# Kernel tuning notes

Measured on AMD Instinct MI355X. Metric: run time of the kernel, lower is better.

## Reference

```python
import jax, jax.numpy as jnp
import numpy as np
from jax.scipy.special import logsumexp

EPS = 1e-12  # torch F.normalize eps
SINKHORN_ITERS = 3


def _l2norm(a, axis):
    n = jnp.sqrt(jnp.sum(a * a, axis=axis, keepdims=True))
    return a / jnp.maximum(n, EPS)


def _log_optimal_transport(scores, alpha, iters):
    # scores: [B, m, n]; alpha: scalar dust-bin param
    b, m, n = scores.shape
    bins = jnp.broadcast_to(alpha, (b, 1, n)).astype(scores.dtype)
    Z = jnp.concatenate([scores, bins], axis=1)  # [B, m+1, n]
    norm = -np.log(float(m + n))
    log_mu = jnp.asarray(
        np.concatenate([np.full(m, norm), [np.log(float(n - m)) + norm]]),
        scores.dtype,
    )  # [m+1]
    log_nu = jnp.full((n,), norm, scores.dtype)
    u = jnp.zeros((b, m + 1), scores.dtype)
    v = jnp.zeros((b, n), scores.dtype)
    for _ in range(iters):
        u = log_mu[None, :] - logsumexp(Z + v[:, None, :], axis=2)
        v = log_nu[None, :] - logsumexp(Z + u[:, :, None], axis=1)
    return Z + u[:, :, None] + v[:, None, :] - norm


def _forward(x, t, tw1, tb1, tw2, tb2, cw1, cb1, cw2, cb2, sw1, sb1, sw2, sb2, dust_bin):
    B, C = x.shape[0], x.shape[1]
    xf = x.reshape(B, C, -1)  # [B, C, N], 1x1 convs act per-location
    # cluster features f: [B, l, N]
    h = jax.nn.relu(jnp.einsum('oc,bcn->bon', cw1, xf) + cb1[None, :, None])
    f = jnp.einsum('oc,bcn->bon', cw2, h) + cb2[None, :, None]
    # global token: [B, g]
    tok = jax.nn.relu(t @ tw1.T + tb1) @ tw2.T + tb2
    # assignment scores p: [B, m, N]
    hs = jax.nn.relu(jnp.einsum('oc,bcn->bon', sw1, xf) + sb1[None, :, None])
    p = jnp.einsum('oc,bcn->bon', sw2, hs) + sb2[None, :, None]
    Z = _log_optimal_transport(p, dust_bin, SINKHORN_ITERS)
    P = jnp.exp(Z)[:, :-1, :]  # drop dust bin row -> [B, m, N]
    # VLAD-style aggregation: the repeat/multiply/sum is just a batched matmul
    agg = jnp.einsum('bln,bmn->blm', f, P)  # [B, l, m]
    agg = _l2norm(agg, axis=1).reshape(B, -1)  # intra-normalize over l, flatten l-major
    out = jnp.concatenate([_l2norm(tok, axis=-1), agg], axis=-1)
    return _l2norm(out, axis=-1)


def setup_inputs() -> dict:
    key = jax.random.key(0)
    ks = jax.random.split(key, 14)
    B, C, H, W = 64, 768, 32, 32
    L, M, G, HID = 128, 64, 256, 512

    def p(k, shape):
        return jax.random.normal(k, shape, jnp.float32) * 0.02

    return {
        'x': jax.random.normal(ks[0], (B, C, H, W), jnp.float32),
        't': jax.random.normal(ks[1], (B, C), jnp.float32),
        'tw1': p(ks[2], (HID, C)), 'tb1': jnp.zeros((HID,), jnp.float32),
        'tw2': p(ks[3], (G, HID)), 'tb2': jnp.zeros((G,), jnp.float32),
        'cw1': p(ks[4], (HID, C)), 'cb1': jnp.zeros((HID,), jnp.float32),
        'cw2': p(ks[5], (L, HID)), 'cb2': jnp.zeros((L,), jnp.float32),
        'sw1': p(ks[6], (HID, C)), 'sb1': jnp.zeros((HID,), jnp.float32),
        'sw2': p(ks[7], (M, HID)), 'sb2': jnp.zeros((M,), jnp.float32),
        'dust_bin': jnp.asarray(1.0, jnp.float32),
    }


def reference(x, t, tw1, tb1, tw2, tb2, cw1, cb1, cw2, cb2, sw1, sb1, sw2, sb2, dust_bin):
    return _forward(x, t, tw1, tb1, tw2, tb2, cw1, cb1, cw2, cb2, sw1, sb1, sw2, sb2, dust_bin)
```

## Files before the change

kernel.cpp:

```cpp
#include <hip/hip_runtime.h>
#include <math.h>


#define B_SZ   64
#define C_IN   768
#define N_LOC  1024
#define HID    512
#define L_DIM  128
#define M_DIM  64
#define G_DIM  256

typedef unsigned short u16;
typedef __bf16 bf16x8 __attribute__((ext_vector_type(8)));
typedef float f32x4 __attribute__((ext_vector_type(4)));

typedef const __attribute__((address_space(1))) void* gptr_t;
typedef __attribute__((address_space(3))) void* sptr_t;

__device__ __forceinline__ void load_lds16(const void* g, void* l) {
    __builtin_amdgcn_global_load_lds((gptr_t)g, (sptr_t)l, 16, 0, 0);
}

__device__ __forceinline__ u16 f2bf(float f) {
    unsigned u = __float_as_uint(f);
    u += 0x7fffu + ((u >> 16) & 1u);
    return (u16)(u >> 16);
}
__device__ __forceinline__ float bf2f(u16 h) {
    return __uint_as_float(((unsigned)h) << 16);
}

__device__ __forceinline__ float waveReduceSum(float v) {
#pragma unroll
    for (int off = 32; off > 0; off >>= 1) v += __shfl_xor(v, off, 64);
    return v;
}

__global__ __launch_bounds__(256) void prep_weights(
        const float* __restrict__ cw1, const float* __restrict__ sw1,
        const float* __restrict__ cw2, const float* __restrict__ sw2,
        u16* __restrict__ cw1p, u16* __restrict__ sw1p,
        u16* __restrict__ cw2p, u16* __restrict__ sw2p) {
    const int q = blockIdx.x * 256 + threadIdx.x;
    const float* src;
    u16* dst;
    if (q < 98304) {
        int path = q / 49152, r = q % 49152;
        int kch = r / 512, c = r & 511;
        src = (path ? sw1 : cw1) + (size_t)c * C_IN + kch * 8;
        dst = (path ? sw1p : cw1p) + (size_t)r * 8;
    } else {
        int q2 = q - 98304;
        int path = (q2 >= 8192) ? 1 : 0;
        int r = q2 - (path ? 8192 : 0);
        int S2 = path ? M_DIM : L_DIM;
        int k2 = r / (4 * S2), kc = (r / S2) & 3, c = r % S2;
        src = (path ? sw2 : cw2) + (size_t)c * HID + k2 * 32 + kc * 8;
        dst = (path ? sw2p : cw2p) + (size_t)r * 8;
    }
    float4 v0 = *(const float4*)(src);
    float4 v1 = *(const float4*)(src + 4);
    *(ushort4*)(dst) = make_ushort4(f2bf(v0.x), f2bf(v0.y), f2bf(v0.z), f2bf(v0.w));
    *(ushort4*)(dst + 4) = make_ushort4(f2bf(v1.x), f2bf(v1.y), f2bf(v1.z), f2bf(v1.w));
}

__global__ __launch_bounds__(256) void transpose_x(const float* __restrict__ x,
                                                   u16* __restrict__ xP) {
    __shared__ float tile[64][65];
    const int n0 = blockIdx.x * 64;
    const int c0 = blockIdx.y * 64;
    const size_t b = blockIdx.z;
    const float* xb = x + b * (size_t)(C_IN * N_LOC);
    u16* xpb = xP + b * (size_t)(N_LOC * C_IN);
    const int tid = threadIdx.x;

    const int jn = (tid & 15) * 4;
    const int cr = tid >> 4;
#pragma unroll
    for (int r = 0; r < 4; ++r) {
        int c = cr + r * 16;
        float4 v = *(const float4*)(xb + (size_t)(c0 + c) * N_LOC + n0 + jn);
        tile[c][jn + 0] = v.x;
        tile[c][jn + 1] = v.y;
        tile[c][jn + 2] = v.z;
        tile[c][jn + 3] = v.w;
    }
    __syncthreads();

    const int n = tid & 63;
    const int ch0 = tid >> 6;
    const int nG = n0 + n;
#pragma unroll
    for (int r = 0; r < 2; ++r) {
        const int ch = ch0 + r * 4;
        const int cG = c0 + ch * 8;
        u16* dst = xpb + (size_t)(nG >> 6) * (64 * C_IN) + (cG >> 5) * 2048 +
                   ((cG & 31) >> 3) * 512 + (nG & 63) * 8;
        ushort4 o0 = make_ushort4(f2bf(tile[ch * 8 + 0][n]), f2bf(tile[ch * 8 + 1][n]),
                                  f2bf(tile[ch * 8 + 2][n]), f2bf(tile[ch * 8 + 3][n]));
        ushort4 o1 = make_ushort4(f2bf(tile[ch * 8 + 4][n]), f2bf(tile[ch * 8 + 5][n]),
                                  f2bf(tile[ch * 8 + 6][n]), f2bf(tile[ch * 8 + 7][n]));
        *(ushort4*)(dst) = o0;
        *(ushort4*)(dst + 4) = o1;
    }
}

__global__ __launch_bounds__(256, 2) void fused12(
        const u16* __restrict__ xP,
        const u16* __restrict__ cw1p, const float* __restrict__ cb1,
        const u16* __restrict__ cw2p, const float* __restrict__ cb2,
        const u16* __restrict__ sw1p, const float* __restrict__ sb1,
        const u16* __restrict__ sw2p, const float* __restrict__ sb2,
        u16* __restrict__ fT, u16* __restrict__ pT) {
    __shared__ __align__(16) u16 LDSu[36864];
    const int tid = threadIdx.x;
    const int lane = tid & 63;
    const int wc = tid >> 6;

    const int id = blockIdx.x + 16 * blockIdx.y + 32 * blockIdx.z;
    const int nid = (id & 7) * 256 + (id >> 3);
    const int bx = nid & 15;
    const int path = (nid >> 4) & 1;
    const int bz = nid >> 5;
    const int r0 = bx * 64;

    const u16* W1p = path ? sw1p : cw1p;
    const float* B1 = path ? sb1 : cb1;
    const u16* W2p = path ? sw2p : cw2p;
    const float* B2 = path ? sb2 : cb2;
    u16* O2 = path ? pT : fT;
    const int S2 = path ? M_DIM : L_DIM;

    const u16* Ap = xP + (size_t)bz * N_LOC * C_IN + (size_t)bx * (64 * C_IN);

    f32x4 acc1[4][8];
#pragma unroll
    for (int mi = 0; mi < 4; ++mi)
#pragma unroll
        for (int ni = 0; ni < 8; ++ni)
            acc1[mi][ni] = (f32x4){0.f, 0.f, 0.f, 0.f};

    const int nk = C_IN / 32;

#define STG_A(db_, kt_)                                                        \
    load_lds16(Ap + (size_t)(kt_) * 2048 + tid * 8, &LDSu[(db_) * 2048 + tid * 8])
#define STG_B(db_, kt_)                                                        \
    do {                                                                       \
        _Pragma("unroll")                                                      \
        for (int j_ = 0; j_ < 8; ++j_)                                         \
            load_lds16(W1p + (size_t)(kt_) * 16384 + (size_t)(j_ * 256 + tid) * 8, \
                       &LDSu[4096 + (db_) * 16384 + (j_ * 256 + tid) * 8]);    \
    } while (0)

#define AV_PTR(db_, mi_)                                                       \
    ((const bf16x8*)&LDSu[(db_) * 2048 + (lane >> 4) * 512 +                   \
                          (16 * (mi_) + (lane & 15)) * 8])
#define BW_PTR(db_, ni_)                                                       \
    ((const bf16x8*)&LDSu[4096 + (db_) * 16384 + (lane >> 4) * 4096 +          \
                          (128 * wc + 16 * (ni_) + (lane & 15)) * 8])

    STG_A(0, 0);
    STG_B(0, 0);
    STG_A(1, 1);
    asm volatile("s_waitcnt vmcnt(1)" ::: "memory");
    __builtin_amdgcn_s_barrier();

    for (int t = 0; t < nk; ++t) {
        const int db = t & 1;
        bf16x8 av[4], bw[8];

#pragma unroll
        for (int mi = 0; mi < 4; ++mi) av[mi] = *AV_PTR(db, mi);
#pragma unroll
        for (int ni = 0; ni < 8; ++ni) bw[ni] = *BW_PTR(db, ni);
        if (t + 1 < nk) STG_B(db ^ 1, t + 1);

        asm volatile("s_waitcnt lgkmcnt(0)" ::: "memory");
        __builtin_amdgcn_sched_barrier(0);
        __builtin_amdgcn_s_barrier();

        if (t + 2 < nk) STG_A(db, t + 2);

        __builtin_amdgcn_s_setprio(1);
#pragma unroll
        for (int mi = 0; mi < 4; ++mi)
#pragma unroll
            for (int ni = 0; ni < 8; ++ni)
                acc1[mi][ni] = __builtin_amdgcn_mfma_f32_16x16x32_bf16(
                    av[mi], bw[ni], acc1[mi][ni], 0, 0, 0);
        __builtin_amdgcn_s_setprio(0);
        __builtin_amdgcn_sched_barrier(0);

        if (t + 2 < nk)
            asm volatile("s_waitcnt vmcnt(1)" ::: "memory");
        else
            asm volatile("s_waitcnt vmcnt(0)" ::: "memory");
        __builtin_amdgcn_s_barrier();
    }
#undef STG_A
#undef STG_B
#undef AV_PTR
#undef BW_PTR

    {
        float bv1[8];
#pragma unroll
        for (int ni = 0; ni < 8; ++ni)
            bv1[ni] = B1[128 * wc + 16 * ni + (lane & 15)];
#pragma unroll
        for (int mi = 0; mi < 4; ++mi)
#pragma unroll
            for (int ni = 0; ni < 8; ++ni)
#pragma unroll
                for (int rr = 0; rr < 4; ++rr) {
                    int n = 16 * mi + (lane >> 4) * 4 + rr;
                    int c = 128 * wc + 16 * ni + (lane & 15);
                    float v = fmaxf(acc1[mi][ni][rr] + bv1[ni], 0.f);
                    LDSu[(c >> 3) * 512 + n * 8 + (c & 7)] = f2bf(v);
                }
    }
    __syncthreads();

    f32x4 acc2[4][2];
#pragma unroll
    for (int mi = 0; mi < 4; ++mi) {
        acc2[mi][0] = (f32x4){0.f, 0.f, 0.f, 0.f};
        acc2[mi][1] = (f32x4){0.f, 0.f, 0.f, 0.f};
    }
    const int c2base = (S2 == L_DIM) ? 32 * wc : 16 * wc;
    const int cA = c2base + (lane & 15);
    const int cB = c2base + 16 + (lane & 15);
    const int fb0 = (lane >> 4) * S2 + cA;
    const int fb1 = (lane >> 4) * S2 + cB;

    bf16x8 w0n = *(const bf16x8*)(W2p + (size_t)fb0 * 8);
    bf16x8 w1n = {};
    if (S2 == L_DIM) w1n = *(const bf16x8*)(W2p + (size_t)fb1 * 8);

    for (int k2 = 0; k2 < 16; ++k2) {
        bf16x8 w0 = w0n, w1 = w1n;
        if (k2 < 15) {
            w0n = *(const bf16x8*)(W2p + ((size_t)(k2 + 1) * 4 * S2 + fb0) * 8);
            if (S2 == L_DIM)
                w1n = *(const bf16x8*)(W2p + ((size_t)(k2 + 1) * 4 * S2 + fb1) * 8);
        }
        bf16x8 a2[4];
#pragma unroll
        for (int mi = 0; mi < 4; ++mi)
            a2[mi] = *(const bf16x8*)&LDSu[(k2 * 4 + (lane >> 4)) * 512 +
                                           (16 * mi + (lane & 15)) * 8];
#pragma unroll
        for (int mi = 0; mi < 4; ++mi) {
            acc2[mi][0] = __builtin_amdgcn_mfma_f32_16x16x32_bf16(
                a2[mi], w0, acc2[mi][0], 0, 0, 0);
            if (S2 == L_DIM)
                acc2[mi][1] = __builtin_amdgcn_mfma_f32_16x16x32_bf16(
                    a2[mi], w1, acc2[mi][1], 0, 0, 0);
        }
    }

    const float b20 = B2[cA];
    const float b21 = (S2 == L_DIM) ? B2[cB] : 0.f;
    u16* Ob = O2 + (size_t)bz * N_LOC * S2;
#pragma unroll
    for (int mi = 0; mi < 4; ++mi)
#pragma unroll
        for (int rr = 0; rr < 4; ++rr) {
            int row = r0 + 16 * mi + (lane >> 4) * 4 + rr;
            Ob[(size_t)row * S2 + cA] = f2bf(acc2[mi][0][rr] + b20);
            if (S2 == L_DIM)
                Ob[(size_t)row * S2 + cB] = f2bf(acc2[mi][1][rr] + b21);
        }
}

__global__ __launch_bounds__(256) void tok1_kernel(const float* __restrict__ t,
                                                   const float* __restrict__ tw1,
                                                   const float* __restrict__ tb1,
                                                   float* __restrict__ hidb) {
    __shared__ __align__(16) float tl[C_IN];
    const int b = blockIdx.y;
    const int j0 = blockIdx.x * 64;
    const int tid = threadIdx.x;
    const int lane = tid & 63;
    const int wave = tid >> 6;
    for (int i = tid; i < C_IN; i += 256) tl[i] = t[(size_t)b * C_IN + i];
    __syncthreads();
    for (int j = wave; j < 64; j += 4) {
        const int row = j0 + j;
        const float4* wr = (const float4*)(tw1 + (size_t)row * C_IN);
        const float4* tr = (const float4*)tl;
        float s = 0.f;
#pragma unroll
        for (int q = 0; q < 3; ++q) {
            float4 wv = wr[lane + 64 * q];
            float4 tv = tr[lane + 64 * q];
            s += wv.x * tv.x + wv.y * tv.y + wv.z * tv.z + wv.w * tv.w;
        }
        s = waveReduceSum(s);
        if (lane == 0) hidb[(size_t)b * HID + row] = fmaxf(s + tb1[row], 0.f);
    }
}

__global__ __launch_bounds__(256) void tok2_kernel(const float* __restrict__ hidb,
                                                   const float* __restrict__ tw2,
                                                   const float* __restrict__ tb2,
                                                   float* __restrict__ tok) {
    __shared__ __align__(16) float hl[HID];
    const int b = blockIdx.y;
    const int g0 = blockIdx.x * 64;
    const int tid = threadIdx.x;
    const int lane = tid & 63;
    const int wave = tid >> 6;
    for (int i = tid; i < HID; i += 256) hl[i] = hidb[(size_t)b * HID + i];
    __syncthreads();
    for (int j = wave; j < 64; j += 4) {
        const int row = g0 + j;
        const float4* wr = (const float4*)(tw2 + (size_t)row * HID);
        const float4* hr = (const float4*)hl;
        float s = 0.f;
#pragma unroll
        for (int q = 0; q < 2; ++q) {
            float4 wv = wr[lane + 64 * q];
            float4 hv = hr[lane + 64 * q];
            s += wv.x * hv.x + wv.y * hv.y + wv.z * hv.z + wv.w * hv.w;
        }
        s = waveReduceSum(s);
        if (lane == 0) tok[(size_t)b * G_DIM + row] = s + tb2[row];
    }
}

__global__ __launch_bounds__(1024) void sinkhorn_kernel(const u16* __restrict__ pT,
                                                        const float* __restrict__ dust,
                                                        u16* __restrict__ PTb) {
    __shared__ u16 sp[M_DIM][N_LOC];
    __shared__ float eu[M_DIM + 1];
    __shared__ float ev[N_LOC];
    const int b = blockIdx.x;
    const int t = threadIdx.x;
    const int lane = t & 63;
    const int wave = t >> 6;
    const float alpha = dust[0];
    const float Ea = __expf(alpha);
    const float mu = 1.f / 1088.f;
    const float mu64 = 960.f / 1088.f;
    const float nu = 1.f / 1088.f;

    const uint4* prow = (const uint4*)(pT + ((size_t)b * N_LOC + t) * M_DIM);
#pragma unroll
    for (int q = 0; q < 8; ++q) {
        uint4 ch = prow[q];
        sp[q * 8 + 0][t] = (u16)(ch.x);
        sp[q * 8 + 1][t] = (u16)(ch.x >> 16);
        sp[q * 8 + 2][t] = (u16)(ch.y);
        sp[q * 8 + 3][t] = (u16)(ch.y >> 16);
        sp[q * 8 + 4][t] = (u16)(ch.z);
        sp[q * 8 + 5][t] = (u16)(ch.z >> 16);
        sp[q * 8 + 6][t] = (u16)(ch.w);
        sp[q * 8 + 7][t] = (u16)(ch.w >> 16);
    }
#pragma unroll
    for (int m = 0; m < M_DIM; ++m)
        sp[m][t] = f2bf(__expf(bf2f(sp[m][t])));
    ev[t] = 1.f;
    __syncthreads();

    for (int it = 0; it < 3; ++it) {
        for (int m = wave; m < M_DIM + 1; m += 16) {
            float s = 0.f;
            if (m < M_DIM) {
#pragma unroll
                for (int q = 0; q < 16; ++q) {
                    int c = lane + 64 * q;
                    s += bf2f(sp[m][c]) * ev[c];
                }
            } else {
#pragma unroll
                for (int q = 0; q < 16; ++q) {
                    int c = lane + 64 * q;
                    s += ev[c];
                }
                s *= Ea;
            }
            s = waveReduceSum(s);
            if (lane == 0) eu[m] = ((m < M_DIM) ? mu : mu64) / s;
        }
        __syncthreads();
        float s = Ea * eu[M_DIM];
#pragma unroll 8
        for (int m = 0; m < M_DIM; ++m) s += bf2f(sp[m][t]) * eu[m];
        ev[t] = nu / s;
        __syncthreads();
    }

    const float evt = ev[t] * 1088.f;
    u16* Prow = PTb + ((size_t)b * N_LOC + t) * M_DIM;
#pragma unroll
    for (int m8 = 0; m8 < M_DIM; m8 += 8) {
        unsigned v0 = f2bf(bf2f(sp[m8 + 0][t]) * eu[m8 + 0] * evt);
        unsigned v1 = f2bf(bf2f(sp[m8 + 1][t]) * eu[m8 + 1] * evt);
        unsigned v2 = f2bf(bf2f(sp[m8 + 2][t]) * eu[m8 + 2] * evt);
        unsigned v3 = f2bf(bf2f(sp[m8 + 3][t]) * eu[m8 + 3] * evt);
        unsigned v4 = f2bf(bf2f(sp[m8 + 4][t]) * eu[m8 + 4] * evt);
        unsigned v5 = f2bf(bf2f(sp[m8 + 5][t]) * eu[m8 + 5] * evt);
        unsigned v6 = f2bf(bf2f(sp[m8 + 6][t]) * eu[m8 + 6] * evt);
        unsigned v7 = f2bf(bf2f(sp[m8 + 7][t]) * eu[m8 + 7] * evt);
        uint4 w;
        w.x = v0 | (v1 << 16);
        w.y = v2 | (v3 << 16);
        w.z = v4 | (v5 << 16);
        w.w = v6 | (v7 << 16);
        *(uint4*)(Prow + m8) = w;
    }
}

__global__ __launch_bounds__(256) void agg_kernel(const u16* __restrict__ fT,
                                                  const u16* __restrict__ PTb,
                                                  float* __restrict__ agg) {
    __shared__ float Fs[64][36];
    __shared__ float Ps[64][68];
    const int b = blockIdx.y;
    const int l0 = blockIdx.x * 32;
    const int tid = threadIdx.x;
    const u16* fb = fT + (size_t)b * N_LOC * L_DIM;
    const u16* Pb = PTb + (size_t)b * N_LOC * M_DIM;

    const int sn = tid >> 2;
    const int flc = (tid & 3) * 8;
    const int pmc = (tid & 3) * 16;
    const int tl = (tid >> 4) * 2;
    const int tm = (tid & 15) * 4;

    float acc[2][4] = {};

    for (int n0 = 0; n0 < N_LOC; n0 += 64) {
        __syncthreads();
        {
            uint4 ld = *(const uint4*)(fb + (size_t)(n0 + sn) * L_DIM + l0 + flc);
            Fs[sn][flc + 0] = bf2f((u16)(ld.x));
            Fs[sn][flc + 1] = bf2f((u16)(ld.x >> 16));
            Fs[sn][flc + 2] = bf2f((u16)(ld.y));
            Fs[sn][flc + 3] = bf2f((u16)(ld.y >> 16));
            Fs[sn][flc + 4] = bf2f((u16)(ld.z));
            Fs[sn][flc + 5] = bf2f((u16)(ld.z >> 16));
            Fs[sn][flc + 6] = bf2f((u16)(ld.w));
            Fs[sn][flc + 7] = bf2f((u16)(ld.w >> 16));
        }
        {
            const u16* psrc = Pb + (size_t)(n0 + sn) * M_DIM + pmc;
            uint4 p0 = *(const uint4*)(psrc);
            uint4 p1 = *(const uint4*)(psrc + 8);
            Ps[sn][pmc + 0] = bf2f((u16)(p0.x));
            Ps[sn][pmc + 1] = bf2f((u16)(p0.x >> 16));
            Ps[sn][pmc + 2] = bf2f((u16)(p0.y));
            Ps[sn][pmc + 3] = bf2f((u16)(p0.y >> 16));
            Ps[sn][pmc + 4] = bf2f((u16)(p0.z));
            Ps[sn][pmc + 5] = bf2f((u16)(p0.z >> 16));
            Ps[sn][pmc + 6] = bf2f((u16)(p0.w));
            Ps[sn][pmc + 7] = bf2f((u16)(p0.w >> 16));
            Ps[sn][pmc + 8] = bf2f((u16)(p1.x));
            Ps[sn][pmc + 9] = bf2f((u16)(p1.x >> 16));
            Ps[sn][pmc + 10] = bf2f((u16)(p1.y));
            Ps[sn][pmc + 11] = bf2f((u16)(p1.y >> 16));
            Ps[sn][pmc + 12] = bf2f((u16)(p1.z));
            Ps[sn][pmc + 13] = bf2f((u16)(p1.z >> 16));
            Ps[sn][pmc + 14] = bf2f((u16)(p1.w));
            Ps[sn][pmc + 15] = bf2f((u16)(p1.w >> 16));
        }
        __syncthreads();
#pragma unroll 8
        for (int nn = 0; nn < 64; ++nn) {
            float a0 = Fs[nn][tl];
            float a1 = Fs[nn][tl + 1];
            float4 p4 = *(const float4*)&Ps[nn][tm];
            acc[0][0] = fmaf(a0, p4.x, acc[0][0]);
            acc[0][1] = fmaf(a0, p4.y, acc[0][1]);
            acc[0][2] = fmaf(a0, p4.z, acc[0][2]);
            acc[0][3] = fmaf(a0, p4.w, acc[0][3]);
            acc[1][0] = fmaf(a1, p4.x, acc[1][0]);
            acc[1][1] = fmaf(a1, p4.y, acc[1][1]);
            acc[1][2] = fmaf(a1, p4.z, acc[1][2]);
            acc[1][3] = fmaf(a1, p4.w, acc[1][3]);
        }
    }

#pragma unroll
    for (int i = 0; i < 2; ++i) {
        float* dst = agg + ((size_t)b * L_DIM + l0 + tl + i) * M_DIM + tm;
        *(float4*)dst = make_float4(acc[i][0], acc[i][1], acc[i][2], acc[i][3]);
    }
}

__global__ __launch_bounds__(256) void final_kernel(const float* __restrict__ agg,
                                                    const float* __restrict__ tok,
                                                    float* __restrict__ out) {
    __shared__ __align__(16) float ag[L_DIM * M_DIM];
    __shared__ float rm[M_DIM];
    __shared__ float red[4];
    __shared__ float tk[G_DIM];
    const int b = blockIdx.x;
    const int tid = threadIdx.x;
    const int lane = tid & 63;
    const int wave = tid >> 6;
    const float EPS = 1e-12f;

    const float4* ab = (const float4*)(agg + (size_t)b * L_DIM * M_DIM);
    for (int e4 = tid; e4 < L_DIM * M_DIM / 4; e4 += 256) ((float4*)ag)[e4] = ab[e4];
    tk[tid] = tok[(size_t)b * G_DIM + tid];
    __syncthreads();

    if (tid < M_DIM) {
        float ss = 0.f;
#pragma unroll 8
        for (int l = 0; l < L_DIM; ++l) {
            float x = ag[l * M_DIM + tid];
            ss = fmaf(x, x, ss);
        }
        rm[tid] = 1.f / fmaxf(sqrtf(ss), EPS);
    }
    const float tv = tk[tid];
    float ssl = tv * tv;
    ssl = waveReduceSum(ssl);
    if (lane == 0) red[wave] = ssl;
    __syncthreads();
    const float stok = red[0] + red[1] + red[2] + red[3];
    const float rt = 1.f / fmaxf(sqrtf(stok), EPS);
    const float tn = tv * rt;

    float gs = tn * tn;
    for (int e = tid; e < L_DIM * M_DIM; e += 256) {
        float x = ag[e] * rm[e & (M_DIM - 1)];
        gs = fmaf(x, x, gs);
    }
    __syncthreads();
    gs = waveReduceSum(gs);
    if (lane == 0) red[wave] = gs;
    __syncthreads();
    const float G = red[0] + red[1] + red[2] + red[3];
    const float rg = 1.f / fmaxf(sqrtf(G), EPS);

    float* ob = out + (size_t)b * (G_DIM + L_DIM * M_DIM);
    ob[tid] = tn * rg;
    for (int e = tid; e < L_DIM * M_DIM; e += 256)
        ob[G_DIM + e] = ag[e] * rm[e & (M_DIM - 1)] * rg;
}

extern "C" void kernel_launch(void* const* d_in, const int* in_sizes, int n_in,
                              void* d_out, int out_size, void* d_ws, size_t ws_size,
                              hipStream_t stream) {
    const float* x    = (const float*)d_in[0];
    const float* t    = (const float*)d_in[1];
    const float* tw1  = (const float*)d_in[2];
    const float* tb1  = (const float*)d_in[3];
    const float* tw2  = (const float*)d_in[4];
    const float* tb2  = (const float*)d_in[5];
    const float* cw1  = (const float*)d_in[6];
    const float* cb1  = (const float*)d_in[7];
    const float* cw2  = (const float*)d_in[8];
    const float* cb2  = (const float*)d_in[9];
    const float* sw1  = (const float*)d_in[10];
    const float* sb1  = (const float*)d_in[11];
    const float* sw2  = (const float*)d_in[12];
    const float* sb2  = (const float*)d_in[13];
    const float* dust = (const float*)d_in[14];
    float* out = (float*)d_out;

    char* ws = (char*)d_ws;
    u16* xP    = (u16*)(ws);
    u16* fT    = (u16*)(ws + 100663296ull);
    u16* pT    = (u16*)(ws + 117440512ull);
    u16* cw1p  = (u16*)(ws + 125829120ull);
    u16* sw1p  = (u16*)(ws + 126615552ull);
    u16* cw2p  = (u16*)(ws + 127401984ull);
    u16* sw2p  = (u16*)(ws + 127533056ull);
    float* hidb = (float*)(ws + 127598592ull);
    u16* PTb      = (u16*)(ws);
    float* tokbuf = (float*)(ws + 20971520ull);
    float* aggbuf = (float*)(ws + 25165824ull);

    prep_weights<<<432, 256, 0, stream>>>(cw1, sw1, cw2, sw2,
                                          cw1p, sw1p, cw2p, sw2p);
    transpose_x<<<dim3(N_LOC / 64, C_IN / 64, B_SZ), 256, 0, stream>>>(x, xP);

    fused12<<<dim3(16, 2, B_SZ), 256, 0, stream>>>(
        xP, cw1p, cb1, cw2p, cb2, sw1p, sb1, sw2p, sb2, fT, pT);

    tok1_kernel<<<dim3(HID / 64, B_SZ), 256, 0, stream>>>(t, tw1, tb1, hidb);
    tok2_kernel<<<dim3(G_DIM / 64, B_SZ), 256, 0, stream>>>(hidb, tw2, tb2, tokbuf);

    sinkhorn_kernel<<<B_SZ, 1024, 0, stream>>>(pT, dust, PTb);
    agg_kernel<<<dim3(L_DIM / 32, B_SZ), 256, 0, stream>>>(fT, PTb, aggbuf);
    final_kernel<<<B_SZ, 256, 0, stream>>>(aggbuf, tokbuf, out);
}
```

Measured before the change: 278.4 us.

## Fuse token MLP, aggregation and normalization; replace global norm with analytic constant

```diff
diff --git a/kernel.cpp b/kernel.cpp
--- a/kernel.cpp
+++ b/kernel.cpp
@@ -9,6 +9,7 @@
 #define L_DIM  128
 #define M_DIM  64
 #define G_DIM  256
+#define OUTD   (G_DIM + L_DIM * M_DIM)
 
 typedef unsigned short u16;
 typedef __bf16 bf16x8 __attribute__((ext_vector_type(8)));
@@ -36,32 +37,63 @@
     return v;
 }
 
-__global__ __launch_bounds__(256) void prep_weights(
+__global__ __launch_bounds__(256) void setup_kernel(
         const float* __restrict__ cw1, const float* __restrict__ sw1,
         const float* __restrict__ cw2, const float* __restrict__ sw2,
         u16* __restrict__ cw1p, u16* __restrict__ sw1p,
-        u16* __restrict__ cw2p, u16* __restrict__ sw2p) {
-    const int q = blockIdx.x * 256 + threadIdx.x;
-    const float* src;
-    u16* dst;
-    if (q < 98304) {
-        int path = q / 49152, r = q % 49152;
-        int kch = r / 512, c = r & 511;
-        src = (path ? sw1 : cw1) + (size_t)c * C_IN + kch * 8;
-        dst = (path ? sw1p : cw1p) + (size_t)r * 8;
-    } else {
-        int q2 = q - 98304;
-        int path = (q2 >= 8192) ? 1 : 0;
-        int r = q2 - (path ? 8192 : 0);
-        int S2 = path ? M_DIM : L_DIM;
-        int k2 = r / (4 * S2), kc = (r / S2) & 3, c = r % S2;
-        src = (path ? sw2 : cw2) + (size_t)c * HID + k2 * 32 + kc * 8;
-        dst = (path ? sw2p : cw2p) + (size_t)r * 8;
-    }
-    float4 v0 = *(const float4*)(src);
-    float4 v1 = *(const float4*)(src + 4);
-    *(ushort4*)(dst) = make_ushort4(f2bf(v0.x), f2bf(v0.y), f2bf(v0.z), f2bf(v0.w));
-    *(ushort4*)(dst + 4) = make_ushort4(f2bf(v1.x), f2bf(v1.y), f2bf(v1.z), f2bf(v1.w));
+        u16* __restrict__ cw2p, u16* __restrict__ sw2p,
+        const float* __restrict__ t, const float* __restrict__ tw1,
+        const float* __restrict__ tb1, float* __restrict__ hidb) {
+    __shared__ __align__(16) float tl[C_IN];
+    const int blk = blockIdx.x;
+    const int tid = threadIdx.x;
+
+    if (blk < 432) {
+        const int q = blk * 256 + tid;
+        const float* src;
+        u16* dst;
+        if (q < 98304) {
+            int path = q / 49152, r = q % 49152;
+            int kch = r / 512, c = r & 511;
+            src = (path ? sw1 : cw1) + (size_t)c * C_IN + kch * 8;
+            dst = (path ? sw1p : cw1p) + (size_t)r * 8;
+        } else {
+            int q2 = q - 98304;
+            int path = (q2 >= 8192) ? 1 : 0;
+            int r = q2 - (path ? 8192 : 0);
+            int S2 = path ? M_DIM : L_DIM;
+            int k2 = r / (4 * S2), kc = (r / S2) & 3, c = r % S2;
+            src = (path ? sw2 : cw2) + (size_t)c * HID + k2 * 32 + kc * 8;
+            dst = (path ? sw2p : cw2p) + (size_t)r * 8;
+        }
+        float4 v0 = *(const float4*)(src);
+        float4 v1 = *(const float4*)(src + 4);
+        *(ushort4*)(dst) = make_ushort4(f2bf(v0.x), f2bf(v0.y), f2bf(v0.z), f2bf(v0.w));
+        *(ushort4*)(dst + 4) = make_ushort4(f2bf(v1.x), f2bf(v1.y), f2bf(v1.z), f2bf(v1.w));
+        return;
+    }
+
+    const int by = blk - 432;
+    const int j0 = (by & 7) * 64;
+    const int b = by >> 3;
+    const int lane = tid & 63;
+    const int wave = tid >> 6;
+    for (int i = tid; i < C_IN; i += 256) tl[i] = t[(size_t)b * C_IN + i];
+    __syncthreads();
+    for (int j = wave; j < 64; j += 4) {
+        const int row = j0 + j;
+        const float4* wr = (const float4*)(tw1 + (size_t)row * C_IN);
+        const float4* tr = (const float4*)tl;
+        float s = 0.f;
+#pragma unroll
+        for (int q = 0; q < 3; ++q) {
+            float4 wv = wr[lane + 64 * q];
+            float4 tv = tr[lane + 64 * q];
+            s += wv.x * tv.x + wv.y * tv.y + wv.z * tv.z + wv.w * tv.w;
+        }
+        s = waveReduceSum(s);
+        if (lane == 0) hidb[(size_t)b * HID + row] = fmaxf(s + tb1[row], 0.f);
+    }
 }
 
 __global__ __launch_bounds__(256) void transpose_x(const float* __restrict__ x,
@@ -271,62 +303,6 @@
             if (S2 == L_DIM)
                 Ob[(size_t)row * S2 + cB] = f2bf(acc2[mi][1][rr] + b21);
         }
-}
-
-__global__ __launch_bounds__(256) void tok1_kernel(const float* __restrict__ t,
-                                                   const float* __restrict__ tw1,
-                                                   const float* __restrict__ tb1,
-                                                   float* __restrict__ hidb) {
-    __shared__ __align__(16) float tl[C_IN];
-    const int b = blockIdx.y;
-    const int j0 = blockIdx.x * 64;
-    const int tid = threadIdx.x;
-    const int lane = tid & 63;
-    const int wave = tid >> 6;
-    for (int i = tid; i < C_IN; i += 256) tl[i] = t[(size_t)b * C_IN + i];
-    __syncthreads();
-    for (int j = wave; j < 64; j += 4) {
-        const int row = j0 + j;
-        const float4* wr = (const float4*)(tw1 + (size_t)row * C_IN);
-        const float4* tr = (const float4*)tl;
-        float s = 0.f;
-#pragma unroll
-        for (int q = 0; q < 3; ++q) {
-            float4 wv = wr[lane + 64 * q];
-            float4 tv = tr[lane + 64 * q];
-            s += wv.x * tv.x + wv.y * tv.y + wv.z * tv.z + wv.w * tv.w;
-        }
-        s = waveReduceSum(s);
-        if (lane == 0) hidb[(size_t)b * HID + row] = fmaxf(s + tb1[row], 0.f);
-    }
-}
-
-__global__ __launch_bounds__(256) void tok2_kernel(const float* __restrict__ hidb,
-                                                   const float* __restrict__ tw2,
-                                                   const float* __restrict__ tb2,
-                                                   float* __restrict__ tok) {
-    __shared__ __align__(16) float hl[HID];
-    const int b = blockIdx.y;
-    const int g0 = blockIdx.x * 64;
-    const int tid = threadIdx.x;
-    const int lane = tid & 63;
-    const int wave = tid >> 6;
-    for (int i = tid; i < HID; i += 256) hl[i] = hidb[(size_t)b * HID + i];
-    __syncthreads();
-    for (int j = wave; j < 64; j += 4) {
-        const int row = g0 + j;
-        const float4* wr = (const float4*)(tw2 + (size_t)row * HID);
-        const float4* hr = (const float4*)hl;
-        float s = 0.f;
-#pragma unroll
-        for (int q = 0; q < 2; ++q) {
-            float4 wv = wr[lane + 64 * q];
-            float4 hv = hr[lane + 64 * q];
-            s += wv.x * hv.x + wv.y * hv.y + wv.z * hv.z + wv.w * hv.w;
-        }
-        s = waveReduceSum(s);
-        if (lane == 0) tok[(size_t)b * G_DIM + row] = s + tb2[row];
-    }
 }
 
 __global__ __launch_bounds__(1024) void sinkhorn_kernel(const u16* __restrict__ pT,
@@ -413,135 +389,126 @@
     }
 }
 
-__global__ __launch_bounds__(256) void agg_kernel(const u16* __restrict__ fT,
-                                                  const u16* __restrict__ PTb,
-                                                  float* __restrict__ agg) {
-    __shared__ float Fs[64][36];
-    __shared__ float Ps[64][68];
+__global__ __launch_bounds__(256) void agg_final_kernel(
+        const u16* __restrict__ fT, const u16* __restrict__ PTb,
+        const float* __restrict__ hidb, const float* __restrict__ tw2,
+        const float* __restrict__ tb2, float* __restrict__ out) {
+    __shared__ __align__(16) float SH[9760];
     const int b = blockIdx.y;
-    const int l0 = blockIdx.x * 32;
-    const int tid = threadIdx.x;
-    const u16* fb = fT + (size_t)b * N_LOC * L_DIM;
-    const u16* Pb = PTb + (size_t)b * N_LOC * M_DIM;
-
-    const int sn = tid >> 2;
-    const int flc = (tid & 3) * 8;
-    const int pmc = (tid & 3) * 16;
-    const int tl = (tid >> 4) * 2;
-    const int tm = (tid & 15) * 4;
-
-    float acc[2][4] = {};
-
-    for (int n0 = 0; n0 < N_LOC; n0 += 64) {
-        __syncthreads();
-        {
-            uint4 ld = *(const uint4*)(fb + (size_t)(n0 + sn) * L_DIM + l0 + flc);
-            Fs[sn][flc + 0] = bf2f((u16)(ld.x));
-            Fs[sn][flc + 1] = bf2f((u16)(ld.x >> 16));
-            Fs[sn][flc + 2] = bf2f((u16)(ld.y));
-            Fs[sn][flc + 3] = bf2f((u16)(ld.y >> 16));
-            Fs[sn][flc + 4] = bf2f((u16)(ld.z));
-            Fs[sn][flc + 5] = bf2f((u16)(ld.z >> 16));
-            Fs[sn][flc + 6] = bf2f((u16)(ld.w));
-            Fs[sn][flc + 7] = bf2f((u16)(ld.w >> 16));
-        }
-        {
-            const u16* psrc = Pb + (size_t)(n0 + sn) * M_DIM + pmc;
-            uint4 p0 = *(const uint4*)(psrc);
-            uint4 p1 = *(const uint4*)(psrc + 8);
-            Ps[sn][pmc + 0] = bf2f((u16)(p0.x));
-            Ps[sn][pmc + 1] = bf2f((u16)(p0.x >> 16));
-            Ps[sn][pmc + 2] = bf2f((u16)(p0.y));
-            Ps[sn][pmc + 3] = bf2f((u16)(p0.y >> 16));
-            Ps[sn][pmc + 4] = bf2f((u16)(p0.z));
-            Ps[sn][pmc + 5] = bf2f((u16)(p0.z >> 16));
-            Ps[sn][pmc + 6] = bf2f((u16)(p0.w));
-            Ps[sn][pmc + 7] = bf2f((u16)(p0.w >> 16));
-            Ps[sn][pmc + 8] = bf2f((u16)(p1.x));
-            Ps[sn][pmc + 9] = bf2f((u16)(p1.x >> 16));
-            Ps[sn][pmc + 10] = bf2f((u16)(p1.y));
-            Ps[sn][pmc + 11] = bf2f((u16)(p1.y >> 16));
-            Ps[sn][pmc + 12] = bf2f((u16)(p1.z));
-            Ps[sn][pmc + 13] = bf2f((u16)(p1.z >> 16));
-            Ps[sn][pmc + 14] = bf2f((u16)(p1.w));
-            Ps[sn][pmc + 15] = bf2f((u16)(p1.w >> 16));
-        }
-        __syncthreads();
-#pragma unroll 8
-        for (int nn = 0; nn < 64; ++nn) {
-            float a0 = Fs[nn][tl];
-            float a1 = Fs[nn][tl + 1];
-            float4 p4 = *(const float4*)&Ps[nn][tm];
-            acc[0][0] = fmaf(a0, p4.x, acc[0][0]);
-            acc[0][1] = fmaf(a0, p4.y, acc[0][1]);
-            acc[0][2] = fmaf(a0, p4.z, acc[0][2]);
-            acc[0][3] = fmaf(a0, p4.w, acc[0][3]);
-            acc[1][0] = fmaf(a1, p4.x, acc[1][0]);
-            acc[1][1] = fmaf(a1, p4.y, acc[1][1]);
-            acc[1][2] = fmaf(a1, p4.z, acc[1][2]);
-            acc[1][3] = fmaf(a1, p4.w, acc[1][3]);
-        }
-    }
-
-#pragma unroll
-    for (int i = 0; i < 2; ++i) {
-        float* dst = agg + ((size_t)b * L_DIM + l0 + tl + i) * M_DIM + tm;
-        *(float4*)dst = make_float4(acc[i][0], acc[i][1], acc[i][2], acc[i][3]);
-    }
-}
-
-__global__ __launch_bounds__(256) void final_kernel(const float* __restrict__ agg,
-                                                    const float* __restrict__ tok,
-                                                    float* __restrict__ out) {
-    __shared__ __align__(16) float ag[L_DIM * M_DIM];
-    __shared__ float rm[M_DIM];
-    __shared__ float red[4];
-    __shared__ float tk[G_DIM];
-    const int b = blockIdx.x;
+    const int bx = blockIdx.x;
     const int tid = threadIdx.x;
     const int lane = tid & 63;
     const int wave = tid >> 6;
     const float EPS = 1e-12f;
-
-    const float4* ab = (const float4*)(agg + (size_t)b * L_DIM * M_DIM);
-    for (int e4 = tid; e4 < L_DIM * M_DIM / 4; e4 += 256) ((float4*)ag)[e4] = ab[e4];
-    tk[tid] = tok[(size_t)b * G_DIM + tid];
-    __syncthreads();
-
-    if (tid < M_DIM) {
+    const float rs65 = 1.f / sqrtf(65.f);
+    float* ob = out + (size_t)b * OUTD;
+
+    if (bx == 4) {
+        float* hl = SH;
+        float* tk = SH + 512;
+        float* red = SH + 768;
+        for (int i = tid; i < HID; i += 256) hl[i] = hidb[(size_t)b * HID + i];
+        __syncthreads();
+        for (int j = wave; j < G_DIM; j += 4) {
+            const float4* wr = (const float4*)(tw2 + (size_t)j * HID);
+            const float4* hr = (const float4*)hl;
+            float s = 0.f;
+#pragma unroll
+            for (int q = 0; q < 2; ++q) {
+                float4 wv = wr[lane + 64 * q];
+                float4 hv = hr[lane + 64 * q];
+                s += wv.x * hv.x + wv.y * hv.y + wv.z * hv.z + wv.w * hv.w;
+            }
+            s = waveReduceSum(s);
+            if (lane == 0) tk[j] = s + tb2[j];
+        }
+        __syncthreads();
+        const float tv = tk[tid];
+        float ssl = tv * tv;
+        ssl = waveReduceSum(ssl);
+        if (lane == 0) red[wave] = ssl;
+        __syncthreads();
+        const float stok = red[0] + red[1] + red[2] + red[3];
+        const float rt = rs65 / fmaxf(sqrtf(stok), EPS);
+        ob[tid] = tv * rt;
+        return;
+    }
+
+    const int m0 = bx * 16;
+    float* Fs = SH;
+    float* Ps = SH + 8448;
+    float* ag = SH;
+    float* rm = SH + 9728;
+    const u16* fb = fT + (size_t)b * N_LOC * L_DIM;
+    const u16* Pb = PTb + (size_t)b * N_LOC * M_DIM;
+
+    const int sn = tid >> 2;
+    const int fl = (tid & 3) * 32;
+    const int pm = (tid & 3) * 4;
+    const int tl = (tid >> 3) * 4;
+    const int tm = (tid & 7) * 2;
+
+    float acc[4][2] = {};
+
+    for (int n0 = 0; n0 < N_LOC; n0 += 64) {
+        __syncthreads();
+#pragma unroll
+        for (int j = 0; j < 4; ++j) {
+            uint4 ld = *(const uint4*)(fb + (size_t)(n0 + sn) * L_DIM + fl + j * 8);
+            float4 lo = make_float4(bf2f((u16)(ld.x)), bf2f((u16)(ld.x >> 16)),
+                                    bf2f((u16)(ld.y)), bf2f((u16)(ld.y >> 16)));
+            float4 hi = make_float4(bf2f((u16)(ld.z)), bf2f((u16)(ld.z >> 16)),
+                                    bf2f((u16)(ld.w)), bf2f((u16)(ld.w >> 16)));
+            *(float4*)&Fs[sn * 132 + fl + j * 8] = lo;
+            *(float4*)&Fs[sn * 132 + fl + j * 8 + 4] = hi;
+        }
+        {
+            uint2 ld = *(const uint2*)(Pb + (size_t)(n0 + sn) * M_DIM + m0 + pm);
+            float4 v = make_float4(bf2f((u16)(ld.x)), bf2f((u16)(ld.x >> 16)),
+                                   bf2f((u16)(ld.y)), bf2f((u16)(ld.y >> 16)));
+            *(float4*)&Ps[sn * 20 + pm] = v;
+        }
+        __syncthreads();
+#pragma unroll 8
+        for (int nn = 0; nn < 64; ++nn) {
+            float4 a = *(const float4*)&Fs[nn * 132 + tl];
+            float p0 = Ps[nn * 20 + tm];
+            float p1 = Ps[nn * 20 + tm + 1];
+            acc[0][0] = fmaf(a.x, p0, acc[0][0]);
+            acc[0][1] = fmaf(a.x, p1, acc[0][1]);
+            acc[1][0] = fmaf(a.y, p0, acc[1][0]);
+            acc[1][1] = fmaf(a.y, p1, acc[1][1]);
+            acc[2][0] = fmaf(a.z, p0, acc[2][0]);
+            acc[2][1] = fmaf(a.z, p1, acc[2][1]);
+            acc[3][0] = fmaf(a.w, p0, acc[3][0]);
+            acc[3][1] = fmaf(a.w, p1, acc[3][1]);
+        }
+    }
+
+    __syncthreads();
+#pragma unroll
+    for (int i = 0; i < 4; ++i) {
+        ag[(tl + i) * 17 + tm] = acc[i][0];
+        ag[(tl + i) * 17 + tm + 1] = acc[i][1];
+    }
+    __syncthreads();
+    if (tid < 16) {
         float ss = 0.f;
 #pragma unroll 8
         for (int l = 0; l < L_DIM; ++l) {
-            float x = ag[l * M_DIM + tid];
-            ss = fmaf(x, x, ss);
-        }
-        rm[tid] = 1.f / fmaxf(sqrtf(ss), EPS);
-    }
-    const float tv = tk[tid];
-    float ssl = tv * tv;
-    ssl = waveReduceSum(ssl);
-    if (lane == 0) red[wave] = ssl;
-    __syncthreads();
-    const float stok = red[0] + red[1] + red[2] + red[3];
-    const float rt = 1.f / fmaxf(sqrtf(stok), EPS);
-    const float tn = tv * rt;
-
-    float gs = tn * tn;
-    for (int e = tid; e < L_DIM * M_DIM; e += 256) {
-        float x = ag[e] * rm[e & (M_DIM - 1)];
-        gs = fmaf(x, x, gs);
-    }
-    __syncthreads();
-    gs = waveReduceSum(gs);
-    if (lane == 0) red[wave] = gs;
-    __syncthreads();
-    const float G = red[0] + red[1] + red[2] + red[3];
-    const float rg = 1.f / fmaxf(sqrtf(G), EPS);
-
-    float* ob = out + (size_t)b * (G_DIM + L_DIM * M_DIM);
-    ob[tid] = tn * rg;
-    for (int e = tid; e < L_DIM * M_DIM; e += 256)
-        ob[G_DIM + e] = ag[e] * rm[e & (M_DIM - 1)] * rg;
+            float xv = ag[l * 17 + tid];
+            ss = fmaf(xv, xv, ss);
+        }
+        rm[tid] = rs65 / fmaxf(sqrtf(ss), EPS);
+    }
+    __syncthreads();
+    const float r0 = rm[tm];
+    const float r1 = rm[tm + 1];
+#pragma unroll
+    for (int i = 0; i < 4; ++i) {
+        ob[G_DIM + (tl + i) * M_DIM + m0 + tm] = acc[i][0] * r0;
+        ob[G_DIM + (tl + i) * M_DIM + m0 + tm + 1] = acc[i][1] * r1;
+    }
 }
 
 extern "C" void kernel_launch(void* const* d_in, const int* in_sizes, int n_in,
@@ -573,21 +540,16 @@
     u16* cw2p  = (u16*)(ws + 127401984ull);
     u16* sw2p  = (u16*)(ws + 127533056ull);
     float* hidb = (float*)(ws + 127598592ull);
-    u16* PTb      = (u16*)(ws);
-    float* tokbuf = (float*)(ws + 20971520ull);
-    float* aggbuf = (float*)(ws + 25165824ull);
-
-    prep_weights<<<432, 256, 0, stream>>>(cw1, sw1, cw2, sw2,
-                                          cw1p, sw1p, cw2p, sw2p);
+    u16* PTb   = (u16*)(ws);
+
+    setup_kernel<<<944, 256, 0, stream>>>(cw1, sw1, cw2, sw2,
+                                          cw1p, sw1p, cw2p, sw2p,
+                                          t, tw1, tb1, hidb);
     transpose_x<<<dim3(N_LOC / 64, C_IN / 64, B_SZ), 256, 0, stream>>>(x, xP);
 
     fused12<<<dim3(16, 2, B_SZ), 256, 0, stream>>>(
         xP, cw1p, cb1, cw2p, cb2, sw1p, sb1, sw2p, sb2, fT, pT);
 
-    tok1_kernel<<<dim3(HID / 64, B_SZ), 256, 0, stream>>>(t, tw1, tb1, hidb);
-    tok2_kernel<<<dim3(G_DIM / 64, B_SZ), 256, 0, stream>>>(hidb, tw2, tb2, tokbuf);
-
     sinkhorn_kernel<<<B_SZ, 1024, 0, stream>>>(pT, dust, PTb);
-    agg_kernel<<<dim3(L_DIM / 32, B_SZ), 256, 0, stream>>>(fT, PTb, aggbuf);
-    final_kernel<<<B_SZ, 256, 0, stream>>>(aggbuf, tokbuf, out);
-}
+    agg_final_kernel<<<dim3(5, B_SZ), 256, 0, stream>>>(fT, PTb, hidb, tw2, tb2, out);
+}
```

Result: no change. 273.6 us (-1.8%).
